# Kernel optimization log

Measured on AMD Instinct MI355X. Metric: run time of the kernel, lower is better.

Reference implementation:

```python
import math
import jax, jax.numpy as jnp
import numpy as np

B, N, C, H = 64, 197, 768, 12
KEEP_RATE = 0.7

def setup_inputs() -> dict:
    key = jax.random.key(0)
    k0, k1, k2 = jax.random.split(key, 3)
    x = jax.random.normal(k0, (B, N, C), jnp.float32)
    qkv_w = jax.random.normal(k1, (C, 3 * C), jnp.float32) * 0.02
    qkv_b = jnp.zeros((3 * C,), jnp.float32)
    proj_w = jax.random.normal(k2, (C, C), jnp.float32) * 0.02
    proj_b = jnp.zeros((C,), jnp.float32)
    return {"x": x, "qkv_w": qkv_w, "qkv_b": qkv_b, "proj_w": proj_w, "proj_b": proj_b}

def reference(x, qkv_w, qkv_b, proj_w, proj_b):
    b, n, c = x.shape
    d = c // H
    scale = d ** -0.5
    # qkv: [B,N,3C] -> [3,B,H,N,d]
    qkv = (x @ qkv_w + qkv_b).reshape(b, n, 3, H, d)
    qkv = jnp.transpose(qkv, (2, 0, 3, 1, 4))
    q, k, v = qkv[0], qkv[1], qkv[2]
    attn = jax.nn.softmax(jnp.einsum('bhnd,bhmd->bhnm', q, k) * scale, axis=-1)  # [B,H,N,N]
    out = jnp.einsum('bhnm,bhmd->bhnd', attn, v)          # [B,H,N,d]
    out = jnp.transpose(out, (0, 2, 1, 3)).reshape(b, n, c)
    x_out = out @ proj_w + proj_b                          # [B,N,C]
    # dynamic token pruning via CLS attention (row 0, excluding CLS itself)
    left_tokens = math.ceil(KEEP_RATE * (n - 1))
    cls_attn = attn[:, :, 0, 1:].mean(axis=1)              # [B,N-1]
    _, idx = jax.lax.top_k(cls_attn, left_tokens)          # descending, sorted
    index = jnp.broadcast_to(idx[:, :, None], (b, left_tokens, c))
    return (x_out, index, idx, cls_attn, left_tokens)
```

## Files before the change

kernel.cpp:

```cpp
#include <hip/hip_runtime.h>
#include <math.h>

#define BB   64
#define NTOK 197
#define CC   768
#define HH   12
#define DH   64
#define MTOT (BB * NTOK)
#define MPAD 12672
#define LEFT 138

#define XOUT_OFF  0
#define INDEX_OFF 9682944
#define IDX_OFF   16465920
#define CLS_OFF   16474752
#define LT_OFF    16487296

typedef short s8v __attribute__((ext_vector_type(8)));
typedef short s4v __attribute__((ext_vector_type(4)));
typedef float f4v __attribute__((ext_vector_type(4)));

#define GLOAD16(g, l) __builtin_amdgcn_global_load_lds( \
    (const __attribute__((address_space(1))) unsigned int*)(g), \
    (__attribute__((address_space(3))) unsigned int*)(l), 16, 0, 0)

__device__ __forceinline__ unsigned short f2bf(float f) {
    union { float f; unsigned int i; } x; x.f = f;
    unsigned int r = x.i + 0x7FFFu + ((x.i >> 16) & 1u);
    return (unsigned short)(r >> 16);
}

__global__ __launch_bounds__(256)
void convert_x(const float* __restrict__ in, unsigned short* __restrict__ outb)
{
    size_t i = ((size_t)blockIdx.x * 256 + threadIdx.x) * 8;
    float4 a = *(const float4*)(in + i);
    float4 b = *(const float4*)(in + i + 4);
    s8v r;
    r[0] = (short)f2bf(a.x); r[1] = (short)f2bf(a.y);
    r[2] = (short)f2bf(a.z); r[3] = (short)f2bf(a.w);
    r[4] = (short)f2bf(b.x); r[5] = (short)f2bf(b.y);
    r[6] = (short)f2bf(b.z); r[7] = (short)f2bf(b.w);
    *(s8v*)(outb + i) = r;
}

__global__ __launch_bounds__(256)
void transpose_w2(const float* __restrict__ inq, const float* __restrict__ inp,
                  unsigned short* __restrict__ outq, unsigned short* __restrict__ outp)
{
    __shared__ float tile[32][33];
    const int bi = blockIdx.x;
    int bj = blockIdx.y;
    const float* in; unsigned short* outb; int N;
    if (bj < 72) { in = inq; outb = outq; N = 2304; }
    else         { bj -= 72; in = inp; outb = outp; N = 768; }
    const int tx = threadIdx.x & 31, ty = threadIdx.x >> 5;
#pragma unroll
    for (int r = ty; r < 32; r += 8)
        tile[r][tx] = in[(size_t)(bi * 32 + r) * N + bj * 32 + tx];
    __syncthreads();
#pragma unroll
    for (int r = ty; r < 32; r += 8)
        outb[(size_t)(bj * 32 + r) * 768 + bi * 32 + tx] = f2bf(tile[tx][r]);
}

__global__ __launch_bounds__(256, 3)
void gemm_bf16(const unsigned short* __restrict__ A, const unsigned short* __restrict__ BT,
               const float* __restrict__ bias, int ncolt, int mode,
               unsigned short* __restrict__ outb, float* __restrict__ outf)
{
    const int id = blockIdx.x;
    const int xcd = id & 7;
    const int t = id >> 3;
    const int ct = t % ncolt, s = t / ncolt;
    const int rt = s * 8 + xcd;
    if (rt >= 99) return;
    const int m0 = rt * 128, n0 = ct * 128;

    const int tid = threadIdx.x;
    const int wave = tid >> 6, lane = tid & 63;
    const int quad = lane >> 4, l16 = lane & 15;
    const int rowbase = (wave >> 1) * 64, colbase = (wave & 1) * 64;
    __shared__ __align__(16) short As[128 * 64];
    __shared__ __align__(16) short Bs[128 * 64];

    const int rA   = lane >> 3;
    const int gcol = ((lane & 7) ^ rA) * 8;
    unsigned int agof[4], bgof[4];
#pragma unroll
    for (int i = 0; i < 4; ++i) {
        int c = wave * 4 + i;
        agof[i] = (unsigned int)((m0 + c * 8 + rA) * 768 + gcol);
        bgof[i] = (unsigned int)((n0 + c * 8 + rA) * 768 + gcol);
    }
    int aoff[4], boff[4];
#pragma unroll
    for (int i = 0; i < 4; ++i) {
        aoff[i] = (rowbase + i * 16 + l16) * 64 + ((quad ^ (l16 & 7)) * 8);
        boff[i] = (colbase + i * 16 + l16) * 64 + ((quad ^ (l16 & 7)) * 8);
    }

    f4v acc[4][4];
#pragma unroll
    for (int i = 0; i < 4; ++i)
#pragma unroll
        for (int j = 0; j < 4; ++j) acc[i][j] = (f4v)0.f;

    for (int k0 = 0; k0 < 768; k0 += 64) {
#pragma unroll
        for (int i = 0; i < 4; ++i) {
            int c = wave * 4 + i;
            GLOAD16(A  + agof[i] + k0, &As[c * 512]);
            GLOAD16(BT + bgof[i] + k0, &Bs[c * 512]);
        }
        __syncthreads();
#pragma unroll
        for (int ks = 0; ks < 2; ++ks) {
            const int x = ks * 32;
            s8v af[4], bf[4];
#pragma unroll
            for (int i = 0; i < 4; ++i) af[i] = *(const s8v*)&As[aoff[i] ^ x];
#pragma unroll
            for (int j = 0; j < 4; ++j) bf[j] = *(const s8v*)&Bs[boff[j] ^ x];
#pragma unroll
            for (int i = 0; i < 4; ++i)
#pragma unroll
                for (int j = 0; j < 4; ++j)
                    acc[i][j] = __builtin_amdgcn_mfma_f32_16x16x32_bf16(bf[j], af[i], acc[i][j], 0, 0, 0);
        }
        __syncthreads();
    }

    const int ncols = mode ? 768 : 2304;
#pragma unroll
    for (int i = 0; i < 4; ++i) {
        const int m = m0 + rowbase + i * 16 + l16;
        if (m >= MTOT) continue;
#pragma unroll
        for (int j = 0; j < 4; ++j) {
            const int nb = n0 + colbase + j * 16 + quad * 4;
            float4 b4 = *(const float4*)&bias[nb];
            if (mode == 1) {
                float4 r;
                r.x = acc[i][j][0] + b4.x; r.y = acc[i][j][1] + b4.y;
                r.z = acc[i][j][2] + b4.z; r.w = acc[i][j][3] + b4.w;
                *(float4*)(outf + (size_t)m * ncols + nb) = r;
            } else {
                s4v r;
                r[0] = (short)f2bf(acc[i][j][0] + b4.x);
                r[1] = (short)f2bf(acc[i][j][1] + b4.y);
                r[2] = (short)f2bf(acc[i][j][2] + b4.z);
                r[3] = (short)f2bf(acc[i][j][3] + b4.w);
                *(s4v*)(outb + (size_t)m * ncols + nb) = r;
            }
        }
    }
}

#define VTS 224

__global__ __launch_bounds__(256)
void transpose_v(const unsigned short* __restrict__ qkv, unsigned short* __restrict__ vt)
{
    __shared__ short tile[32][33];
    const int bx = blockIdx.x;
    const int by = blockIdx.y;
    const int bh = blockIdx.z;
    const int b = bh / HH, h = bh - b * HH;
    const int tx = threadIdx.x & 31, ty = threadIdx.x >> 5;
    const unsigned short* vin = qkv + (size_t)b * NTOK * 2304 + 1536 + h * DH;
#pragma unroll
    for (int r = ty; r < 32; r += 8) {
        const int tok = bx * 32 + r;
        tile[r][tx] = (tok < NTOK) ? (short)vin[(size_t)tok * 2304 + by * 32 + tx] : (short)0;
    }
    __syncthreads();
#pragma unroll
    for (int r = ty; r < 32; r += 8) {
        const int d = by * 32 + r;
        vt[((size_t)bh * DH + d) * VTS + bx * 32 + tx] = tile[tx][r];
    }
}

#define PSTR 226

__global__ __launch_bounds__(256, 2)
void attn_mfma4(const unsigned short* __restrict__ qkv, const unsigned short* __restrict__ vt,
                unsigned short* __restrict__ attnbf)
{
    const int bh = blockIdx.x;
    const int g  = blockIdx.y;
    const int b = bh / HH, h = bh - b * HH;
    const int tid = threadIdx.x;
    const int wave = tid >> 6, lane = tid & 63;
    const int quad = lane >> 4, l16 = lane & 15;
    __shared__ __align__(16) short Ks[NTOK * 64];
    __shared__ short Ps[4][16 * PSTR];

    const unsigned short* qg = qkv + (size_t)b * NTOK * 2304 + h * DH;
    const unsigned short* kg = qg + 768;
    const unsigned short* vtb = vt + (size_t)bh * DH * VTS;

    for (int u = tid; u < NTOK * 8; u += 256) {
        const int row = u >> 3, seg = u & 7;
        *(s8v*)&Ks[row * 64 + (seg ^ (row & 7)) * 8] =
            *(const s8v*)(kg + (size_t)row * 2304 + seg * 8);
    }
    __syncthreads();

    const int strip = g * 4 + wave;
    if (strip >= 13) return;

    const int mq = min(strip * 16 + l16, NTOK - 1);
    const s8v aq0 = *(const s8v*)(qg + (size_t)mq * 2304 + quad * 8);
    const s8v aq1 = *(const s8v*)(qg + (size_t)mq * 2304 + 32 + quad * 8);

    f4v sacc[14];
#pragma unroll
    for (int j = 0; j < 14; ++j) sacc[j] = (f4v)0.f;
    __builtin_amdgcn_s_setprio(1);
#pragma unroll
    for (int j = 0; j < 14; ++j) {
        const int kt = min(j * 16 + l16, NTOK - 1);
        s8v bk0 = *(const s8v*)&Ks[kt * 64 + ((quad       ^ (kt & 7)) * 8)];
        s8v bk1 = *(const s8v*)&Ks[kt * 64 + (((quad + 4) ^ (kt & 7)) * 8)];
        sacc[j] = __builtin_amdgcn_mfma_f32_16x16x32_bf16(bk0, aq0, sacc[j], 0, 0, 0);
        sacc[j] = __builtin_amdgcn_mfma_f32_16x16x32_bf16(bk1, aq1, sacc[j], 0, 0, 0);
    }
    __builtin_amdgcn_s_setprio(0);

    s8v bvr[7][4];
#pragma unroll
    for (int t = 0; t < 7; ++t) {
        const int ko = t * 32 + quad * 8;
#pragma unroll
        for (int j = 0; j < 4; ++j)
            bvr[t][j] = *(const s8v*)(vtb + (size_t)(j * 16 + l16) * VTS + ko);
    }

    float mx = -1e30f;
#pragma unroll
    for (int j = 0; j < 14; ++j)
#pragma unroll
        for (int r = 0; r < 4; ++r) {
            const int key = j * 16 + quad * 4 + r;
            float s = (key < NTOK) ? sacc[j][r] * 0.125f : -1e30f;
            sacc[j][r] = s;
            mx = fmaxf(mx, s);
        }
    mx = fmaxf(mx, __shfl_xor(mx, 16, 64));
    mx = fmaxf(mx, __shfl_xor(mx, 32, 64));

    float sm = 0.f;
#pragma unroll
    for (int j = 0; j < 14; ++j) {
        s4v pk;
#pragma unroll
        for (int r = 0; r < 4; ++r) {
            const int key = j * 16 + quad * 4 + r;
            float p = (key < NTOK) ? __expf(sacc[j][r] - mx) : 0.f;
            sm += p;
            pk[r] = (short)f2bf(p);
        }
        *(s4v*)&Ps[wave][l16 * PSTR + j * 16 + quad * 4] = pk;
    }
    sm += __shfl_xor(sm, 16, 64);
    sm += __shfl_xor(sm, 32, 64);
    const float rcp = 1.f / sm;

    f4v oacc[4];
#pragma unroll
    for (int j = 0; j < 4; ++j) oacc[j] = (f4v)0.f;
    __builtin_amdgcn_s_setprio(1);
#pragma unroll
    for (int t = 0; t < 7; ++t) {
        const int ko = t * 32 + quad * 8;
        s8v ap = *(const s8v*)&Ps[wave][l16 * PSTR + ko];
#pragma unroll
        for (int j = 0; j < 4; ++j)
            oacc[j] = __builtin_amdgcn_mfma_f32_16x16x32_bf16(bvr[t][j], ap, oacc[j], 0, 0, 0);
    }
    __builtin_amdgcn_s_setprio(0);
    const int qrow = strip * 16 + l16;
    if (qrow < NTOK) {
#pragma unroll
        for (int j = 0; j < 4; ++j) {
            s4v o4;
#pragma unroll
            for (int r = 0; r < 4; ++r) o4[r] = (short)f2bf(oacc[j][r] * rcp);
            *(s4v*)&attnbf[((size_t)b * NTOK + qrow) * 768 + h * DH + j * 16 + quad * 4] = o4;
        }
    }
}

#define QCH  64
#define BGRP 8

__global__ __launch_bounds__(256)
void qr_kernel(const float* __restrict__ x, const float* __restrict__ qkv_w,
               const float* __restrict__ qkv_b, float* __restrict__ rws,
               float* __restrict__ bconst)
{
    const int h  = blockIdx.x;
    const int b0 = blockIdx.y * BGRP;
    const int tid = threadIdx.x;
    __shared__ float x0s[BGRP][CC];
    __shared__ float wbuf[2][QCH * DH];
    __shared__ float q0s[BGRP][DH];

    for (int u = tid; u < BGRP * CC; u += 256) {
        int b = u / CC, c = u - b * CC;
        x0s[b][c] = x[(size_t)(b0 + b) * NTOK * CC + c];
    }
    for (int u = tid; u < QCH * DH; u += 256) {
        int cc = u >> 6, dd = u & 63;
        wbuf[0][u] = qkv_w[(size_t)cc * 2304 + h * DH + dd];
    }
    __syncthreads();

    const int d  = tid & 63;
    const int bA = tid >> 6;
    const int bB = bA + 4;
    float accA = qkv_b[h * DH + d];
    float accB = qkv_b[h * DH + d];
    for (int k = 0; k < CC / QCH; ++k) {
        const int cur = k & 1;
        if (k + 1 < CC / QCH) {
            const int cbase = (k + 1) * QCH;
            for (int u = tid; u < QCH * DH; u += 256) {
                int cc = u >> 6, dd = u & 63;
                wbuf[cur ^ 1][u] = qkv_w[(size_t)(cbase + cc) * 2304 + h * DH + dd];
            }
        }
        const int cb = k * QCH;
#pragma unroll
        for (int cc = 0; cc < QCH; ++cc) {
            const float wv = wbuf[cur][cc * 64 + d];
            accA = fmaf(x0s[bA][cb + cc], wv, accA);
            accB = fmaf(x0s[bB][cb + cc], wv, accB);
        }
        __syncthreads();
    }
    q0s[bA][d] = accA;
    q0s[bB][d] = accB;
    __syncthreads();

    if (tid < BGRP) {
        float acc3 = 0.f;
        for (int dd = 0; dd < DH; ++dd) acc3 += q0s[tid][dd] * qkv_b[CC + h * DH + dd];
        bconst[(b0 + tid) * HH + h] = acc3;
    }

    for (int c = tid; c < CC; c += 256) {
        const float* wrow = qkv_w + (size_t)c * 2304 + CC + h * DH;
        float acc2[BGRP];
#pragma unroll
        for (int b = 0; b < BGRP; ++b) acc2[b] = 0.f;
#pragma unroll
        for (int dd = 0; dd < DH; dd += 4) {
            float4 w4 = *(const float4*)(wrow + dd);
#pragma unroll
            for (int b = 0; b < BGRP; ++b) {
                acc2[b] = fmaf(w4.x, q0s[b][dd + 0], acc2[b]);
                acc2[b] = fmaf(w4.y, q0s[b][dd + 1], acc2[b]);
                acc2[b] = fmaf(w4.z, q0s[b][dd + 2], acc2[b]);
                acc2[b] = fmaf(w4.w, q0s[b][dd + 3], acc2[b]);
            }
        }
#pragma unroll
        for (int b = 0; b < BGRP; ++b)
            rws[((size_t)(b0 + b) * HH + h) * CC + c] = acc2[b];
    }
}

__global__ __launch_bounds__(256)
void cls_s(const float* __restrict__ x, const float* __restrict__ rws,
           const float* __restrict__ bconst, float* __restrict__ sws)
{
    const int b = blockIdx.y;
    const int tid = threadIdx.x;
    __shared__ __align__(16) float rl[HH * 772];
    __shared__ float bcs[HH];
#pragma unroll
    for (int h = 0; h < HH; ++h)
        for (int c = tid; c < CC; c += 256)
            rl[h * 772 + c] = rws[((size_t)b * HH + h) * CC + c];
    if (tid < HH) bcs[tid] = bconst[b * HH + tid];
    __syncthreads();
    const int local = blockIdx.x * 256 + tid;
    if (local < NTOK * HH) {
        const int tok = local / HH;
        const int h = local - tok * HH;
        const float* xr = x + ((size_t)b * NTOK + tok) * CC;
        const float* rp = rl + h * 772;
        float acc = 0.f;
#pragma unroll 8
        for (int c = 0; c < CC; c += 4) {
            float4 x4 = *(const float4*)(xr + c);
            float4 r4 = *(const float4*)(rp + c);
            acc = fmaf(x4.x, r4.x, acc);
            acc = fmaf(x4.y, r4.y, acc);
            acc = fmaf(x4.z, r4.z, acc);
            acc = fmaf(x4.w, r4.w, acc);
        }
        sws[((size_t)b * HH + h) * NTOK + tok] = (acc + bcs[h]) * 0.125f;
    }
}

__global__ __launch_bounds__(256)
void cls_topk(const float* __restrict__ sws, float* __restrict__ out, int write_lt)
{
    const int b = blockIdx.x, tid = threadIdx.x;
    const int wave = tid >> 6, lane = tid & 63;
    __shared__ float sbuf[HH][208];
    __shared__ float pm[4][208];
    __shared__ float vals[256];
    __shared__ int   idxs[256];

    for (int jj = lane; jj < 208; jj += 64) pm[wave][jj] = 0.f;
    if (tid < NTOK) {
#pragma unroll
        for (int h = 0; h < HH; ++h)
            sbuf[h][tid] = sws[((size_t)b * HH + h) * NTOK + tid];
    }
    __syncthreads();

    for (int h = wave; h < HH; h += 4) {
        float sv[4], ev[4];
        float mx = -1e30f;
#pragma unroll
        for (int t = 0; t < 4; ++t) {
            int j = lane + 64 * t;
            sv[t] = (j < NTOK) ? sbuf[h][j] : -1e30f;
            mx = fmaxf(mx, sv[t]);
        }
#pragma unroll
        for (int off = 1; off < 64; off <<= 1) mx = fmaxf(mx, __shfl_xor(mx, off, 64));
        float sm = 0.f;
#pragma unroll
        for (int t = 0; t < 4; ++t) {
            int j = lane + 64 * t;
            ev[t] = (j < NTOK) ? expf(sv[t] - mx) : 0.f;
            sm += ev[t];
        }
#pragma unroll
        for (int off = 1; off < 64; off <<= 1) sm += __shfl_xor(sm, off, 64);
#pragma unroll
        for (int t = 0; t < 4; ++t) {
            int j = lane + 64 * t;
            if (j < NTOK) pm[wave][j] += ev[t] / sm;
        }
    }
    __syncthreads();

    float v = -INFINITY;
    int id = 256 + tid;
    if (tid < NTOK - 1) {
        int j = tid + 1;
        float s = ((pm[0][j] + pm[1][j]) + (pm[2][j] + pm[3][j])) * (1.f / 12.f);
        v = s; id = tid;
        out[CLS_OFF + (size_t)b * (NTOK - 1) + tid] = s;
    }
    vals[tid] = v; idxs[tid] = id;
    __syncthreads();

    for (int k = 2; k <= 256; k <<= 1) {
        for (int j = k >> 1; j > 0; j >>= 1) {
            int ixj = tid ^ j;
            if (ixj > tid) {
                float va = vals[tid], vb2 = vals[ixj];
                int ia = idxs[tid], ib = idxs[ixj];
                bool aLess = (va > vb2) || (va == vb2 && ia < ib);
                bool dir = ((tid & k) == 0);
                if (dir != aLess) {
                    vals[tid] = vb2; vals[ixj] = va;
                    idxs[tid] = ib;  idxs[ixj] = ia;
                }
            }
            __syncthreads();
        }
    }

    if (tid < LEFT) out[IDX_OFF + (size_t)b * LEFT + tid] = (float)idxs[tid];
    if (write_lt && b == 0 && tid == 0) out[LT_OFF] = (float)LEFT;
}

__global__ __launch_bounds__(64)
void write_index(const float* __restrict__ idx_in, float* __restrict__ out)
{
    const int row = blockIdx.x;
    const float v = idx_in[row];
    const int tid = threadIdx.x;
    float4 r; r.x = v; r.y = v; r.z = v; r.w = v;
#pragma unroll
    for (int i = 0; i < 3; ++i)
        *(float4*)(out + INDEX_OFF + (size_t)row * CC + (tid + 64 * i) * 4) = r;
}

extern "C" void kernel_launch(void* const* d_in, const int* in_sizes, int n_in,
                              void* d_out, int out_size, void* d_ws, size_t ws_size,
                              hipStream_t stream)
{
    const float* x      = (const float*)d_in[0];
    const float* qkv_w  = (const float*)d_in[1];
    const float* qkv_b  = (const float*)d_in[2];
    const float* proj_w = (const float*)d_in[3];
    const float* proj_b = (const float*)d_in[4];
    float* out = (float*)d_out;

    char* w = (char*)d_ws;
    unsigned short* xbf   = (unsigned short*)w; w += (size_t)MPAD * CC * 2;
    unsigned short* wt1   = (unsigned short*)w; w += (size_t)3 * CC * CC * 2;
    unsigned short* wt2   = (unsigned short*)w; w += (size_t)CC * CC * 2;
    unsigned short* qkvbf = (unsigned short*)w; w += (size_t)MTOT * 3 * CC * 2;
    unsigned short* atbf  = (unsigned short*)w; w += (size_t)MPAD * CC * 2;
    float* rws    = (float*)w; w += (size_t)BB * HH * CC * 4;
    float* bconst = (float*)w; w += (size_t)BB * HH * 4;
    float* sws    = (float*)w; w += (size_t)BB * HH * NTOK * 4;
    unsigned short* vtbf  = (unsigned short*)d_ws;

    convert_x<<<dim3(4728), 256, 0, stream>>>(x, xbf);
    transpose_w2<<<dim3(24, 96), 256, 0, stream>>>(qkv_w, proj_w, wt1, wt2);
    qr_kernel<<<dim3(HH, BB / BGRP), 256, 0, stream>>>(x, qkv_w, qkv_b, rws, bconst);
    cls_s<<<dim3(10, 64), 256, 0, stream>>>(x, rws, bconst, sws);
    cls_topk<<<dim3(BB), 256, 0, stream>>>(sws, out, (out_size > LT_OFF) ? 1 : 0);
    write_index<<<dim3(BB * LEFT), 64, 0, stream>>>(out + IDX_OFF, out);
    gemm_bf16<<<dim3(8 * 18 * 13), 256, 0, stream>>>(xbf, wt1, qkv_b, 18, 0, qkvbf, nullptr);
    transpose_v<<<dim3(7, 2, BB * HH), 256, 0, stream>>>(qkvbf, vtbf);
    attn_mfma4<<<dim3(BB * HH, 4), 256, 0, stream>>>(qkvbf, vtbf, atbf);
    gemm_bf16<<<dim3(8 * 6 * 13), 256, 0, stream>>>(atbf, wt2, proj_b, 6, 1,
                                                    nullptr, out + XOUT_OFF);
}
```

Measured before the change: 342.7 us.

## Stage x tiles in LDS for CLS scores and split QKV GEMM into two launches

The CLS score kernel now stages chunks of the token rows of x in shared memory with double buffering. Each token's row is then read once from global memory and reused across all 12 heads, instead of each thread reading its own full strided row. The QKV GEMM is also split into two launches covering row tiles 0-49 and 50-98, which changes wave quantization and tail effects. The split adds one launch and changes the grid shape. The cls_s change adds a __syncthreads per chunk.

```diff
diff --git a/kernel.cpp b/kernel.cpp
--- a/kernel.cpp
+++ b/kernel.cpp
@@ -66,7 +66,7 @@
 
 __global__ __launch_bounds__(256, 3)
 void gemm_bf16(const unsigned short* __restrict__ A, const unsigned short* __restrict__ BT,
-               const float* __restrict__ bias, int ncolt, int mode,
+               const float* __restrict__ bias, int ncolt, int mode, int rt0, int nrt,
                unsigned short* __restrict__ outb, float* __restrict__ outf)
 {
     const int id = blockIdx.x;
@@ -74,8 +74,8 @@
     const int t = id >> 3;
     const int ct = t % ncolt, s = t / ncolt;
     const int rt = s * 8 + xcd;
-    if (rt >= 99) return;
-    const int m0 = rt * 128, n0 = ct * 128;
+    if (rt >= nrt) return;
+    const int m0 = (rt0 + rt) * 128, n0 = ct * 128;
 
     const int tid = threadIdx.x;
     const int wave = tid >> 6, lane = tid & 63;
@@ -373,6 +373,10 @@
     }
 }
 
+#define CTOK 22
+#define CCH  96
+#define CSTR 100
+
 __global__ __launch_bounds__(256)
 void cls_s(const float* __restrict__ x, const float* __restrict__ rws,
            const float* __restrict__ bconst, float* __restrict__ sws)
@@ -381,30 +385,61 @@
     const int tid = threadIdx.x;
     __shared__ __align__(16) float rl[HH * 772];
     __shared__ float bcs[HH];
-#pragma unroll
-    for (int h = 0; h < HH; ++h)
-        for (int c = tid; c < CC; c += 256)
-            rl[h * 772 + c] = rws[((size_t)b * HH + h) * CC + c];
+    __shared__ __align__(16) float xt[2][CTOK * CSTR];
+
+    for (int u = tid; u < HH * CC; u += 256) {
+        int h = u / CC, c = u - h * CC;
+        rl[h * 772 + c] = rws[(size_t)b * HH * CC + u];
+    }
     if (tid < HH) bcs[tid] = bconst[b * HH + tid];
-    __syncthreads();
-    const int local = blockIdx.x * 256 + tid;
-    if (local < NTOK * HH) {
-        const int tok = local / HH;
-        const int h = local - tok * HH;
-        const float* xr = x + ((size_t)b * NTOK + tok) * CC;
-        const float* rp = rl + h * 772;
-        float acc = 0.f;
-#pragma unroll 8
-        for (int c = 0; c < CC; c += 4) {
-            float4 x4 = *(const float4*)(xr + c);
-            float4 r4 = *(const float4*)(rp + c);
-            acc = fmaf(x4.x, r4.x, acc);
-            acc = fmaf(x4.y, r4.y, acc);
-            acc = fmaf(x4.z, r4.z, acc);
-            acc = fmaf(x4.w, r4.w, acc);
-        }
+
+    const int pair0 = blockIdx.x * 256;
+    const int tok0 = pair0 / HH;
+    const int local = pair0 + tid;
+    const int tok = local / HH;
+    const int h = local - tok * HH;
+    const bool act = (local < NTOK * HH);
+    const int trow = tok - tok0;
+
+    for (int u = tid; u < CTOK * (CCH / 4); u += 256) {
+        const int row = u / (CCH / 4), c4 = u - row * (CCH / 4);
+        const int tk = tok0 + row;
+        if (tk < NTOK)
+            *(float4*)&xt[0][row * CSTR + c4 * 4] =
+                *(const float4*)(x + ((size_t)b * NTOK + tk) * CC + c4 * 4);
+    }
+    __syncthreads();
+
+    float acc = 0.f;
+    for (int ch = 0; ch < CC / CCH; ++ch) {
+        const int cur = ch & 1;
+        if (ch + 1 < CC / CCH) {
+            const int cb = (ch + 1) * CCH;
+            for (int u = tid; u < CTOK * (CCH / 4); u += 256) {
+                const int row = u / (CCH / 4), c4 = u - row * (CCH / 4);
+                const int tk = tok0 + row;
+                if (tk < NTOK)
+                    *(float4*)&xt[cur ^ 1][row * CSTR + c4 * 4] =
+                        *(const float4*)(x + ((size_t)b * NTOK + tk) * CC + cb + c4 * 4);
+            }
+        }
+        if (act) {
+            const float* xr = &xt[cur][trow * CSTR];
+            const float* rp = rl + h * 772 + ch * CCH;
+#pragma unroll
+            for (int c = 0; c < CCH; c += 4) {
+                float4 x4 = *(const float4*)(xr + c);
+                float4 r4 = *(const float4*)(rp + c);
+                acc = fmaf(x4.x, r4.x, acc);
+                acc = fmaf(x4.y, r4.y, acc);
+                acc = fmaf(x4.z, r4.z, acc);
+                acc = fmaf(x4.w, r4.w, acc);
+            }
+        }
+        __syncthreads();
+    }
+    if (act)
         sws[((size_t)b * HH + h) * NTOK + tok] = (acc + bcs[h]) * 0.125f;
-    }
 }
 
 __global__ __launch_bounds__(256)
@@ -525,9 +560,10 @@
     cls_s<<<dim3(10, 64), 256, 0, stream>>>(x, rws, bconst, sws);
     cls_topk<<<dim3(BB), 256, 0, stream>>>(sws, out, (out_size > LT_OFF) ? 1 : 0);
     write_index<<<dim3(BB * LEFT), 64, 0, stream>>>(out + IDX_OFF, out);
-    gemm_bf16<<<dim3(8 * 18 * 13), 256, 0, stream>>>(xbf, wt1, qkv_b, 18, 0, qkvbf, nullptr);
+    gemm_bf16<<<dim3(8 * 18 * 7), 256, 0, stream>>>(xbf, wt1, qkv_b, 18, 0, 0, 50, qkvbf, nullptr);
+    gemm_bf16<<<dim3(8 * 18 * 7), 256, 0, stream>>>(xbf, wt1, qkv_b, 18, 0, 50, 49, qkvbf, nullptr);
     transpose_v<<<dim3(7, 2, BB * HH), 256, 0, stream>>>(qkvbf, vtbf);
     attn_mfma4<<<dim3(BB * HH, 4), 256, 0, stream>>>(qkvbf, vtbf, atbf);
-    gemm_bf16<<<dim3(8 * 6 * 13), 256, 0, stream>>>(atbf, wt2, proj_b, 6, 1,
+    gemm_bf16<<<dim3(8 * 6 * 13), 256, 0, stream>>>(atbf, wt2, proj_b, 6, 1, 0, 99,
                                                     nullptr, out + XOUT_OFF);
 }
```

After: 353.4 us. +3.1%, slower.

## Merge independent stages into multi-role fused kernels to cut launch count

Applied to the files above, without the earlier changes.

Ten kernel launches are folded into five by dispatching different work on block index: conversion, weight transpose and the CLS query projection share one launch, cls_s rides alongside the QKV GEMM, top-k alongside the V transpose, and index writing alongside the projection GEMM. The qr work is also re-gridded from 8-batch groups per block to one (batch, head) per block, with only one wave doing the first reduction. This removes launch gaps and lets small side tasks overlap with large ones. The cost is larger shared memory per block, which may lower occupancy, and the qr stage now rereads weights per batch.

```diff
diff --git a/kernel.cpp b/kernel.cpp
--- a/kernel.cpp
+++ b/kernel.cpp
@@ -30,10 +30,11 @@
     return (unsigned short)(r >> 16);
 }
 
-__global__ __launch_bounds__(256)
-void convert_x(const float* __restrict__ in, unsigned short* __restrict__ outb)
-{
-    size_t i = ((size_t)blockIdx.x * 256 + threadIdx.x) * 8;
+
+__device__ __forceinline__ void convert_x_body(int blk, int tid,
+        const float* __restrict__ in, unsigned short* __restrict__ outb)
+{
+    size_t i = ((size_t)blk * 256 + tid) * 8;
     float4 a = *(const float4*)(in + i);
     float4 b = *(const float4*)(in + i + 4);
     s8v r;
@@ -44,17 +45,17 @@
     *(s8v*)(outb + i) = r;
 }
 
-__global__ __launch_bounds__(256)
-void transpose_w2(const float* __restrict__ inq, const float* __restrict__ inp,
-                  unsigned short* __restrict__ outq, unsigned short* __restrict__ outp)
-{
-    __shared__ float tile[32][33];
-    const int bi = blockIdx.x;
-    int bj = blockIdx.y;
+__device__ __forceinline__ void transpose_w_body(int q, int tid, char* smem,
+        const float* __restrict__ inq, const float* __restrict__ inp,
+        unsigned short* __restrict__ outq, unsigned short* __restrict__ outp)
+{
+    float (*tile)[33] = (float(*)[33])smem;
+    const int bi = q % 24;
+    int bj = q / 24;
     const float* in; unsigned short* outb; int N;
     if (bj < 72) { in = inq; outb = outq; N = 2304; }
     else         { bj -= 72; in = inp; outb = outp; N = 768; }
-    const int tx = threadIdx.x & 31, ty = threadIdx.x >> 5;
+    const int tx = tid & 31, ty = tid >> 5;
 #pragma unroll
     for (int r = ty; r < 32; r += 8)
         tile[r][tx] = in[(size_t)(bi * 32 + r) * N + bj * 32 + tx];
@@ -64,12 +65,70 @@
         outb[(size_t)(bj * 32 + r) * 768 + bi * 32 + tx] = f2bf(tile[tx][r]);
 }
 
-__global__ __launch_bounds__(256, 3)
-void gemm_bf16(const unsigned short* __restrict__ A, const unsigned short* __restrict__ BT,
-               const float* __restrict__ bias, int ncolt, int mode,
-               unsigned short* __restrict__ outb, float* __restrict__ outf)
-{
-    const int id = blockIdx.x;
+#define QCH 64
+__device__ __forceinline__ void qr_body(int blk, int tid, char* smem,
+        const float* __restrict__ x, const float* __restrict__ qkv_w,
+        const float* __restrict__ qkv_b, float* __restrict__ rws,
+        float* __restrict__ bconst)
+{
+    const int b = blk / HH, h = blk - b * HH;
+    float* x0    = (float*)smem;
+    float* q0h   = (float*)(smem + 3072);
+    float* wbuf0 = (float*)(smem + 3328);
+    float* wbuf1 = (float*)(smem + 19712);
+    for (int c = tid; c < CC; c += 256) x0[c] = x[(size_t)b * NTOK * CC + c];
+    for (int u = tid; u < QCH * DH; u += 256) {
+        int cc = u >> 6, o = u & 63;
+        wbuf0[u] = qkv_w[(size_t)cc * 2304 + h * DH + o];
+    }
+    __syncthreads();
+    float acc = 0.f;
+    if (tid < DH) acc = qkv_b[h * DH + tid];
+    for (int k = 0; k < CC / QCH; ++k) {
+        float* wcur  = (k & 1) ? wbuf1 : wbuf0;
+        float* wnext = (k & 1) ? wbuf0 : wbuf1;
+        if (k + 1 < CC / QCH) {
+            const int cbase = (k + 1) * QCH;
+            for (int u = tid; u < QCH * DH; u += 256) {
+                int cc = u >> 6, o = u & 63;
+                wnext[u] = qkv_w[(size_t)(cbase + cc) * 2304 + h * DH + o];
+            }
+        }
+        if (tid < DH) {
+            const int cbase = k * QCH;
+#pragma unroll
+            for (int cc = 0; cc < QCH; ++cc)
+                acc = fmaf(x0[cbase + cc], wcur[cc * 64 + tid], acc);
+        }
+        __syncthreads();
+    }
+    if (tid < DH) q0h[tid] = acc;
+    __syncthreads();
+    for (int c = tid; c < CC; c += 256) {
+        const float* wrow = qkv_w + (size_t)c * 2304 + CC + h * DH;
+        float acc2 = 0.f;
+#pragma unroll
+        for (int d = 0; d < DH; d += 4) {
+            float4 w4 = *(const float4*)(wrow + d);
+            acc2 = fmaf(w4.x, q0h[d + 0], acc2);
+            acc2 = fmaf(w4.y, q0h[d + 1], acc2);
+            acc2 = fmaf(w4.z, q0h[d + 2], acc2);
+            acc2 = fmaf(w4.w, q0h[d + 3], acc2);
+        }
+        rws[((size_t)b * HH + h) * CC + c] = acc2;
+    }
+    if (tid == 0) {
+        float acc3 = 0.f;
+        for (int d = 0; d < DH; ++d) acc3 += q0h[d] * qkv_b[CC + h * DH + d];
+        bconst[blk] = acc3;
+    }
+}
+
+__device__ __forceinline__ void gemm_body(int id, int tid, char* smem,
+        const unsigned short* __restrict__ A, const unsigned short* __restrict__ BT,
+        const float* __restrict__ bias, int ncolt, int mode,
+        unsigned short* __restrict__ outb, float* __restrict__ outf)
+{
     const int xcd = id & 7;
     const int t = id >> 3;
     const int ct = t % ncolt, s = t / ncolt;
@@ -77,12 +136,11 @@
     if (rt >= 99) return;
     const int m0 = rt * 128, n0 = ct * 128;
 
-    const int tid = threadIdx.x;
     const int wave = tid >> 6, lane = tid & 63;
     const int quad = lane >> 4, l16 = lane & 15;
     const int rowbase = (wave >> 1) * 64, colbase = (wave & 1) * 64;
-    __shared__ __align__(16) short As[128 * 64];
-    __shared__ __align__(16) short Bs[128 * 64];
+    short* As = (short*)smem;
+    short* Bs = (short*)(smem + 16384);
 
     const int rA   = lane >> 3;
     const int gcol = ((lane & 7) ^ rA) * 8;
@@ -157,237 +215,20 @@
     }
 }
 
-#define VTS 224
-
-__global__ __launch_bounds__(256)
-void transpose_v(const unsigned short* __restrict__ qkv, unsigned short* __restrict__ vt)
-{
-    __shared__ short tile[32][33];
-    const int bx = blockIdx.x;
-    const int by = blockIdx.y;
-    const int bh = blockIdx.z;
-    const int b = bh / HH, h = bh - b * HH;
-    const int tx = threadIdx.x & 31, ty = threadIdx.x >> 5;
-    const unsigned short* vin = qkv + (size_t)b * NTOK * 2304 + 1536 + h * DH;
-#pragma unroll
-    for (int r = ty; r < 32; r += 8) {
-        const int tok = bx * 32 + r;
-        tile[r][tx] = (tok < NTOK) ? (short)vin[(size_t)tok * 2304 + by * 32 + tx] : (short)0;
-    }
-    __syncthreads();
-#pragma unroll
-    for (int r = ty; r < 32; r += 8) {
-        const int d = by * 32 + r;
-        vt[((size_t)bh * DH + d) * VTS + bx * 32 + tx] = tile[tx][r];
-    }
-}
-
-#define PSTR 226
-
-__global__ __launch_bounds__(256, 2)
-void attn_mfma4(const unsigned short* __restrict__ qkv, const unsigned short* __restrict__ vt,
-                unsigned short* __restrict__ attnbf)
-{
-    const int bh = blockIdx.x;
-    const int g  = blockIdx.y;
-    const int b = bh / HH, h = bh - b * HH;
-    const int tid = threadIdx.x;
-    const int wave = tid >> 6, lane = tid & 63;
-    const int quad = lane >> 4, l16 = lane & 15;
-    __shared__ __align__(16) short Ks[NTOK * 64];
-    __shared__ short Ps[4][16 * PSTR];
-
-    const unsigned short* qg = qkv + (size_t)b * NTOK * 2304 + h * DH;
-    const unsigned short* kg = qg + 768;
-    const unsigned short* vtb = vt + (size_t)bh * DH * VTS;
-
-    for (int u = tid; u < NTOK * 8; u += 256) {
-        const int row = u >> 3, seg = u & 7;
-        *(s8v*)&Ks[row * 64 + (seg ^ (row & 7)) * 8] =
-            *(const s8v*)(kg + (size_t)row * 2304 + seg * 8);
-    }
-    __syncthreads();
-
-    const int strip = g * 4 + wave;
-    if (strip >= 13) return;
-
-    const int mq = min(strip * 16 + l16, NTOK - 1);
-    const s8v aq0 = *(const s8v*)(qg + (size_t)mq * 2304 + quad * 8);
-    const s8v aq1 = *(const s8v*)(qg + (size_t)mq * 2304 + 32 + quad * 8);
-
-    f4v sacc[14];
-#pragma unroll
-    for (int j = 0; j < 14; ++j) sacc[j] = (f4v)0.f;
-    __builtin_amdgcn_s_setprio(1);
-#pragma unroll
-    for (int j = 0; j < 14; ++j) {
-        const int kt = min(j * 16 + l16, NTOK - 1);
-        s8v bk0 = *(const s8v*)&Ks[kt * 64 + ((quad       ^ (kt & 7)) * 8)];
-        s8v bk1 = *(const s8v*)&Ks[kt * 64 + (((quad + 4) ^ (kt & 7)) * 8)];
-        sacc[j] = __builtin_amdgcn_mfma_f32_16x16x32_bf16(bk0, aq0, sacc[j], 0, 0, 0);
-        sacc[j] = __builtin_amdgcn_mfma_f32_16x16x32_bf16(bk1, aq1, sacc[j], 0, 0, 0);
-    }
-    __builtin_amdgcn_s_setprio(0);
-
-    s8v bvr[7][4];
-#pragma unroll
-    for (int t = 0; t < 7; ++t) {
-        const int ko = t * 32 + quad * 8;
-#pragma unroll
-        for (int j = 0; j < 4; ++j)
-            bvr[t][j] = *(const s8v*)(vtb + (size_t)(j * 16 + l16) * VTS + ko);
-    }
-
-    float mx = -1e30f;
-#pragma unroll
-    for (int j = 0; j < 14; ++j)
-#pragma unroll
-        for (int r = 0; r < 4; ++r) {
-            const int key = j * 16 + quad * 4 + r;
-            float s = (key < NTOK) ? sacc[j][r] * 0.125f : -1e30f;
-            sacc[j][r] = s;
-            mx = fmaxf(mx, s);
-        }
-    mx = fmaxf(mx, __shfl_xor(mx, 16, 64));
-    mx = fmaxf(mx, __shfl_xor(mx, 32, 64));
-
-    float sm = 0.f;
-#pragma unroll
-    for (int j = 0; j < 14; ++j) {
-        s4v pk;
-#pragma unroll
-        for (int r = 0; r < 4; ++r) {
-            const int key = j * 16 + quad * 4 + r;
-            float p = (key < NTOK) ? __expf(sacc[j][r] - mx) : 0.f;
-            sm += p;
-            pk[r] = (short)f2bf(p);
-        }
-        *(s4v*)&Ps[wave][l16 * PSTR + j * 16 + quad * 4] = pk;
-    }
-    sm += __shfl_xor(sm, 16, 64);
-    sm += __shfl_xor(sm, 32, 64);
-    const float rcp = 1.f / sm;
-
-    f4v oacc[4];
-#pragma unroll
-    for (int j = 0; j < 4; ++j) oacc[j] = (f4v)0.f;
-    __builtin_amdgcn_s_setprio(1);
-#pragma unroll
-    for (int t = 0; t < 7; ++t) {
-        const int ko = t * 32 + quad * 8;
-        s8v ap = *(const s8v*)&Ps[wave][l16 * PSTR + ko];
-#pragma unroll
-        for (int j = 0; j < 4; ++j)
-            oacc[j] = __builtin_amdgcn_mfma_f32_16x16x32_bf16(bvr[t][j], ap, oacc[j], 0, 0, 0);
-    }
-    __builtin_amdgcn_s_setprio(0);
-    const int qrow = strip * 16 + l16;
-    if (qrow < NTOK) {
-#pragma unroll
-        for (int j = 0; j < 4; ++j) {
-            s4v o4;
-#pragma unroll
-            for (int r = 0; r < 4; ++r) o4[r] = (short)f2bf(oacc[j][r] * rcp);
-            *(s4v*)&attnbf[((size_t)b * NTOK + qrow) * 768 + h * DH + j * 16 + quad * 4] = o4;
-        }
-    }
-}
-
-#define QCH  64
-#define BGRP 8
-
-__global__ __launch_bounds__(256)
-void qr_kernel(const float* __restrict__ x, const float* __restrict__ qkv_w,
-               const float* __restrict__ qkv_b, float* __restrict__ rws,
-               float* __restrict__ bconst)
-{
-    const int h  = blockIdx.x;
-    const int b0 = blockIdx.y * BGRP;
-    const int tid = threadIdx.x;
-    __shared__ float x0s[BGRP][CC];
-    __shared__ float wbuf[2][QCH * DH];
-    __shared__ float q0s[BGRP][DH];
-
-    for (int u = tid; u < BGRP * CC; u += 256) {
-        int b = u / CC, c = u - b * CC;
-        x0s[b][c] = x[(size_t)(b0 + b) * NTOK * CC + c];
-    }
-    for (int u = tid; u < QCH * DH; u += 256) {
-        int cc = u >> 6, dd = u & 63;
-        wbuf[0][u] = qkv_w[(size_t)cc * 2304 + h * DH + dd];
-    }
-    __syncthreads();
-
-    const int d  = tid & 63;
-    const int bA = tid >> 6;
-    const int bB = bA + 4;
-    float accA = qkv_b[h * DH + d];
-    float accB = qkv_b[h * DH + d];
-    for (int k = 0; k < CC / QCH; ++k) {
-        const int cur = k & 1;
-        if (k + 1 < CC / QCH) {
-            const int cbase = (k + 1) * QCH;
-            for (int u = tid; u < QCH * DH; u += 256) {
-                int cc = u >> 6, dd = u & 63;
-                wbuf[cur ^ 1][u] = qkv_w[(size_t)(cbase + cc) * 2304 + h * DH + dd];
-            }
-        }
-        const int cb = k * QCH;
-#pragma unroll
-        for (int cc = 0; cc < QCH; ++cc) {
-            const float wv = wbuf[cur][cc * 64 + d];
-            accA = fmaf(x0s[bA][cb + cc], wv, accA);
-            accB = fmaf(x0s[bB][cb + cc], wv, accB);
-        }
-        __syncthreads();
-    }
-    q0s[bA][d] = accA;
-    q0s[bB][d] = accB;
-    __syncthreads();
-
-    if (tid < BGRP) {
-        float acc3 = 0.f;
-        for (int dd = 0; dd < DH; ++dd) acc3 += q0s[tid][dd] * qkv_b[CC + h * DH + dd];
-        bconst[(b0 + tid) * HH + h] = acc3;
-    }
-
-    for (int c = tid; c < CC; c += 256) {
-        const float* wrow = qkv_w + (size_t)c * 2304 + CC + h * DH;
-        float acc2[BGRP];
-#pragma unroll
-        for (int b = 0; b < BGRP; ++b) acc2[b] = 0.f;
-#pragma unroll
-        for (int dd = 0; dd < DH; dd += 4) {
-            float4 w4 = *(const float4*)(wrow + dd);
-#pragma unroll
-            for (int b = 0; b < BGRP; ++b) {
-                acc2[b] = fmaf(w4.x, q0s[b][dd + 0], acc2[b]);
-                acc2[b] = fmaf(w4.y, q0s[b][dd + 1], acc2[b]);
-                acc2[b] = fmaf(w4.z, q0s[b][dd + 2], acc2[b]);
-                acc2[b] = fmaf(w4.w, q0s[b][dd + 3], acc2[b]);
-            }
-        }
-#pragma unroll
-        for (int b = 0; b < BGRP; ++b)
-            rws[((size_t)(b0 + b) * HH + h) * CC + c] = acc2[b];
-    }
-}
-
-__global__ __launch_bounds__(256)
-void cls_s(const float* __restrict__ x, const float* __restrict__ rws,
-           const float* __restrict__ bconst, float* __restrict__ sws)
-{
-    const int b = blockIdx.y;
-    const int tid = threadIdx.x;
-    __shared__ __align__(16) float rl[HH * 772];
-    __shared__ float bcs[HH];
+__device__ __forceinline__ void cls_s_body(int q, int tid, char* smem,
+        const float* __restrict__ x, const float* __restrict__ rws,
+        const float* __restrict__ bconst, float* __restrict__ sws)
+{
+    const int bx = q % 10, b = q / 10;
+    float* rl  = (float*)smem;
+    float* bcs = (float*)(smem + 37056);
 #pragma unroll
     for (int h = 0; h < HH; ++h)
         for (int c = tid; c < CC; c += 256)
             rl[h * 772 + c] = rws[((size_t)b * HH + h) * CC + c];
     if (tid < HH) bcs[tid] = bconst[b * HH + tid];
     __syncthreads();
-    const int local = blockIdx.x * 256 + tid;
+    const int local = bx * 256 + tid;
     if (local < NTOK * HH) {
         const int tok = local / HH;
         const int h = local - tok * HH;
@@ -407,15 +248,38 @@
     }
 }
 
-__global__ __launch_bounds__(256)
-void cls_topk(const float* __restrict__ sws, float* __restrict__ out, int write_lt)
-{
-    const int b = blockIdx.x, tid = threadIdx.x;
+#define VTS 224
+__device__ __forceinline__ void transpose_v_body(int q, int tid, char* smem,
+        const unsigned short* __restrict__ qkv, unsigned short* __restrict__ vt)
+{
+    short (*tile)[33] = (short(*)[33])smem;
+    const int bx = q % 7;
+    const int by = (q / 7) & 1;
+    const int bh = q / 14;
+    const int b = bh / HH, h = bh - b * HH;
+    const int tx = tid & 31, ty = tid >> 5;
+    const unsigned short* vin = qkv + (size_t)b * NTOK * 2304 + 1536 + h * DH;
+#pragma unroll
+    for (int r = ty; r < 32; r += 8) {
+        const int tok = bx * 32 + r;
+        tile[r][tx] = (tok < NTOK) ? (short)vin[(size_t)tok * 2304 + by * 32 + tx] : (short)0;
+    }
+    __syncthreads();
+#pragma unroll
+    for (int r = ty; r < 32; r += 8) {
+        const int d = by * 32 + r;
+        vt[((size_t)bh * DH + d) * VTS + bx * 32 + tx] = tile[tx][r];
+    }
+}
+
+__device__ __forceinline__ void cls_topk_body(int b, int tid, char* smem,
+        const float* __restrict__ sws, float* __restrict__ out, int write_lt)
+{
     const int wave = tid >> 6, lane = tid & 63;
-    __shared__ float sbuf[HH][208];
-    __shared__ float pm[4][208];
-    __shared__ float vals[256];
-    __shared__ int   idxs[256];
+    float (*sbuf)[208] = (float(*)[208])smem;
+    float (*pm)[208]   = (float(*)[208])(smem + 9984);
+    float* vals        = (float*)(smem + 13312);
+    int*   idxs        = (int*)(smem + 14336);
 
     for (int jj = lane; jj < 208; jj += 64) pm[wave][jj] = 0.f;
     if (tid < NTOK) {
@@ -485,16 +349,189 @@
     if (write_lt && b == 0 && tid == 0) out[LT_OFF] = (float)LEFT;
 }
 
-__global__ __launch_bounds__(64)
-void write_index(const float* __restrict__ idx_in, float* __restrict__ out)
-{
-    const int row = blockIdx.x;
+__device__ __forceinline__ void write_index_body(int row, int tid,
+        const float* __restrict__ idx_in, float* __restrict__ out)
+{
     const float v = idx_in[row];
+    if (tid < 192) {
+        float4 r; r.x = v; r.y = v; r.z = v; r.w = v;
+        *(float4*)(out + INDEX_OFF + (size_t)row * CC + tid * 4) = r;
+    }
+}
+
+#define PRE_QR 768
+#define PRE_CV 4728
+#define PRE_TW 2304
+
+__global__ __launch_bounds__(256)
+void fat_pre(const float* __restrict__ x, const float* __restrict__ qkv_w,
+             const float* __restrict__ qkv_b, const float* __restrict__ proj_w,
+             unsigned short* __restrict__ xbf, unsigned short* __restrict__ wt1,
+             unsigned short* __restrict__ wt2, float* __restrict__ rws,
+             float* __restrict__ bconst)
+{
+    __shared__ __align__(16) char smem[36096];
+    const int id = blockIdx.x, tid = threadIdx.x;
+    if (id < PRE_QR)
+        qr_body(id, tid, smem, x, qkv_w, qkv_b, rws, bconst);
+    else if (id < PRE_QR + PRE_CV)
+        convert_x_body(id - PRE_QR, tid, x, xbf);
+    else
+        transpose_w_body(id - PRE_QR - PRE_CV, tid, smem, qkv_w, proj_w, wt1, wt2);
+}
+
+#define QKV_GEMM (8 * 18 * 13)
+
+__global__ __launch_bounds__(256, 3)
+void fat_qkv(const unsigned short* __restrict__ xbf, const unsigned short* __restrict__ wt1,
+             const float* __restrict__ qkv_b, unsigned short* __restrict__ qkvbf,
+             const float* __restrict__ x, const float* __restrict__ rws,
+             const float* __restrict__ bconst, float* __restrict__ sws)
+{
+    __shared__ __align__(16) char smem[37104];
+    const int id = blockIdx.x, tid = threadIdx.x;
+    if (id < QKV_GEMM)
+        gemm_body(id, tid, smem, xbf, wt1, qkv_b, 18, 0, qkvbf, nullptr);
+    else
+        cls_s_body(id - QKV_GEMM, tid, smem, x, rws, bconst, sws);
+}
+
+__global__ __launch_bounds__(256)
+void fat_tv(const unsigned short* __restrict__ qkvbf, unsigned short* __restrict__ vt,
+            const float* __restrict__ sws, float* __restrict__ out, int write_lt)
+{
+    __shared__ __align__(16) char smem[15360];
+    const int id = blockIdx.x, tid = threadIdx.x;
+    if (id < 64)
+        cls_topk_body(id, tid, smem, sws, out, write_lt);
+    else
+        transpose_v_body(id - 64, tid, smem, qkvbf, vt);
+}
+
+#define PROJ_GEMM (8 * 6 * 13)
+
+__global__ __launch_bounds__(256, 3)
+void fat_proj(const unsigned short* __restrict__ atbf, const unsigned short* __restrict__ wt2,
+              const float* __restrict__ proj_b, float* __restrict__ outf,
+              const float* __restrict__ idx_in, float* __restrict__ out)
+{
+    __shared__ __align__(16) char smem[32768];
+    const int id = blockIdx.x, tid = threadIdx.x;
+    if (id < PROJ_GEMM)
+        gemm_body(id, tid, smem, atbf, wt2, proj_b, 6, 1, nullptr, outf);
+    else
+        write_index_body(id - PROJ_GEMM, tid, idx_in, out);
+}
+
+#define PSTR 226
+
+__global__ __launch_bounds__(256, 2)
+void attn_mfma4(const unsigned short* __restrict__ qkv, const unsigned short* __restrict__ vt,
+                unsigned short* __restrict__ attnbf)
+{
+    const int bh = blockIdx.x;
+    const int g  = blockIdx.y;
+    const int b = bh / HH, h = bh - b * HH;
     const int tid = threadIdx.x;
-    float4 r; r.x = v; r.y = v; r.z = v; r.w = v;
-#pragma unroll
-    for (int i = 0; i < 3; ++i)
-        *(float4*)(out + INDEX_OFF + (size_t)row * CC + (tid + 64 * i) * 4) = r;
+    const int wave = tid >> 6, lane = tid & 63;
+    const int quad = lane >> 4, l16 = lane & 15;
+    __shared__ __align__(16) short Ks[NTOK * 64];
+    __shared__ short Ps[4][16 * PSTR];
+
+    const unsigned short* qg = qkv + (size_t)b * NTOK * 2304 + h * DH;
+    const unsigned short* kg = qg + 768;
+    const unsigned short* vtb = vt + (size_t)bh * DH * VTS;
+
+    for (int u = tid; u < NTOK * 8; u += 256) {
+        const int row = u >> 3, seg = u & 7;
+        *(s8v*)&Ks[row * 64 + (seg ^ (row & 7)) * 8] =
+            *(const s8v*)(kg + (size_t)row * 2304 + seg * 8);
+    }
+    __syncthreads();
+
+    const int strip = g * 4 + wave;
+    if (strip >= 13) return;
+
+    const int mq = min(strip * 16 + l16, NTOK - 1);
+    const s8v aq0 = *(const s8v*)(qg + (size_t)mq * 2304 + quad * 8);
+    const s8v aq1 = *(const s8v*)(qg + (size_t)mq * 2304 + 32 + quad * 8);
+
+    f4v sacc[14];
+#pragma unroll
+    for (int j = 0; j < 14; ++j) sacc[j] = (f4v)0.f;
+    __builtin_amdgcn_s_setprio(1);
+#pragma unroll
+    for (int j = 0; j < 14; ++j) {
+        const int kt = min(j * 16 + l16, NTOK - 1);
+        s8v bk0 = *(const s8v*)&Ks[kt * 64 + ((quad       ^ (kt & 7)) * 8)];
+        s8v bk1 = *(const s8v*)&Ks[kt * 64 + (((quad + 4) ^ (kt & 7)) * 8)];
+        sacc[j] = __builtin_amdgcn_mfma_f32_16x16x32_bf16(bk0, aq0, sacc[j], 0, 0, 0);
+        sacc[j] = __builtin_amdgcn_mfma_f32_16x16x32_bf16(bk1, aq1, sacc[j], 0, 0, 0);
+    }
+    __builtin_amdgcn_s_setprio(0);
+
+    s8v bvr[7][4];
+#pragma unroll
+    for (int t = 0; t < 7; ++t) {
+        const int ko = t * 32 + quad * 8;
+#pragma unroll
+        for (int j = 0; j < 4; ++j)
+            bvr[t][j] = *(const s8v*)(vtb + (size_t)(j * 16 + l16) * VTS + ko);
+    }
+
+    float mx = -1e30f;
+#pragma unroll
+    for (int j = 0; j < 14; ++j)
+#pragma unroll
+        for (int r = 0; r < 4; ++r) {
+            const int key = j * 16 + quad * 4 + r;
+            float s = (key < NTOK) ? sacc[j][r] * 0.125f : -1e30f;
+            sacc[j][r] = s;
+            mx = fmaxf(mx, s);
+        }
+    mx = fmaxf(mx, __shfl_xor(mx, 16, 64));
+    mx = fmaxf(mx, __shfl_xor(mx, 32, 64));
+
+    float sm = 0.f;
+#pragma unroll
+    for (int j = 0; j < 14; ++j) {
+        s4v pk;
+#pragma unroll
+        for (int r = 0; r < 4; ++r) {
+            const int key = j * 16 + quad * 4 + r;
+            float p = (key < NTOK) ? __expf(sacc[j][r] - mx) : 0.f;
+            sm += p;
+            pk[r] = (short)f2bf(p);
+        }
+        *(s4v*)&Ps[wave][l16 * PSTR + j * 16 + quad * 4] = pk;
+    }
+    sm += __shfl_xor(sm, 16, 64);
+    sm += __shfl_xor(sm, 32, 64);
+    const float rcp = 1.f / sm;
+
+    f4v oacc[4];
+#pragma unroll
+    for (int j = 0; j < 4; ++j) oacc[j] = (f4v)0.f;
+    __builtin_amdgcn_s_setprio(1);
+#pragma unroll
+    for (int t = 0; t < 7; ++t) {
+        const int ko = t * 32 + quad * 8;
+        s8v ap = *(const s8v*)&Ps[wave][l16 * PSTR + ko];
+#pragma unroll
+        for (int j = 0; j < 4; ++j)
+            oacc[j] = __builtin_amdgcn_mfma_f32_16x16x32_bf16(bvr[t][j], ap, oacc[j], 0, 0, 0);
+    }
+    __builtin_amdgcn_s_setprio(0);
+    const int qrow = strip * 16 + l16;
+    if (qrow < NTOK) {
+#pragma unroll
+        for (int j = 0; j < 4; ++j) {
+            s4v o4;
+#pragma unroll
+            for (int r = 0; r < 4; ++r) o4[r] = (short)f2bf(oacc[j][r] * rcp);
+            *(s4v*)&attnbf[((size_t)b * NTOK + qrow) * 768 + h * DH + j * 16 + quad * 4] = o4;
+        }
+    }
 }
 
 extern "C" void kernel_launch(void* const* d_in, const int* in_sizes, int n_in,
@@ -519,15 +556,13 @@
     float* sws    = (float*)w; w += (size_t)BB * HH * NTOK * 4;
     unsigned short* vtbf  = (unsigned short*)d_ws;
 
-    convert_x<<<dim3(4728), 256, 0, stream>>>(x, xbf);
-    transpose_w2<<<dim3(24, 96), 256, 0, stream>>>(qkv_w, proj_w, wt1, wt2);
-    qr_kernel<<<dim3(HH, BB / BGRP), 256, 0, stream>>>(x, qkv_w, qkv_b, rws, bconst);
-    cls_s<<<dim3(10, 64), 256, 0, stream>>>(x, rws, bconst, sws);
-    cls_topk<<<dim3(BB), 256, 0, stream>>>(sws, out, (out_size > LT_OFF) ? 1 : 0);
-    write_index<<<dim3(BB * LEFT), 64, 0, stream>>>(out + IDX_OFF, out);
-    gemm_bf16<<<dim3(8 * 18 * 13), 256, 0, stream>>>(xbf, wt1, qkv_b, 18, 0, qkvbf, nullptr);
-    transpose_v<<<dim3(7, 2, BB * HH), 256, 0, stream>>>(qkvbf, vtbf);
+    fat_pre<<<dim3(PRE_QR + PRE_CV + PRE_TW), 256, 0, stream>>>(
+        x, qkv_w, qkv_b, proj_w, xbf, wt1, wt2, rws, bconst);
+    fat_qkv<<<dim3(QKV_GEMM + 640), 256, 0, stream>>>(
+        xbf, wt1, qkv_b, qkvbf, x, rws, bconst, sws);
+    fat_tv<<<dim3(64 + 7 * 2 * BB * HH), 256, 0, stream>>>(
+        qkvbf, vtbf, sws, out, (out_size > LT_OFF) ? 1 : 0);
     attn_mfma4<<<dim3(BB * HH, 4), 256, 0, stream>>>(qkvbf, vtbf, atbf);
-    gemm_bf16<<<dim3(8 * 6 * 13), 256, 0, stream>>>(atbf, wt2, proj_b, 6, 1,
-                                                    nullptr, out + XOUT_OFF);
-}
+    fat_proj<<<dim3(PROJ_GEMM + BB * LEFT), 256, 0, stream>>>(
+        atbf, wt2, proj_b, out + XOUT_OFF, out + IDX_OFF, out);
+}
```

Result: faster. 311.1 us (-9.2%).
